# Kernel tuning notes

Hardware: AMD Instinct MI355X
Metric: run time of the kernel (lower is better)

The kernel has to match this reference:

```python
import jax, jax.numpy as jnp
import numpy as np

B, SQ, SK = 32, 512, 512
Q_DIM = 512
K_DIM = 512
H = 8
HD = 64
INNER = H * HD
MAX_POS = 512
SCALE = 1.0 / np.sqrt(HD)


def setup_inputs() -> dict:
    key = jax.random.key(0)
    ks = jax.random.split(key, 10)
    query = jax.random.normal(ks[0], (B, SQ, Q_DIM), dtype=jnp.float32)
    key_t = jax.random.normal(ks[1], (B, SK, K_DIM), dtype=jnp.float32)
    value = jax.random.normal(ks[2], (B, SK, K_DIM), dtype=jnp.float32)
    mask = jax.random.randint(ks[3], (B, SQ, SK), 0, 2, dtype=jnp.int32)
    # learned parameters (Linear weights stored as [in, out]; to_q/k/v have no bias)
    Wq = jax.random.normal(ks[4], (Q_DIM, INNER), dtype=jnp.float32) * 0.02
    Wk = jax.random.normal(ks[5], (K_DIM, INNER), dtype=jnp.float32) * 0.02
    Wv = jax.random.normal(ks[6], (K_DIM, INNER), dtype=jnp.float32) * 0.02
    Wo = jax.random.normal(ks[7], (INNER, Q_DIM), dtype=jnp.float32) * 0.02
    bo = jnp.zeros((Q_DIM,), dtype=jnp.float32)
    rel_pos_emb = jax.random.normal(ks[8], (MAX_POS, MAX_POS), dtype=jnp.float32) * 0.02
    return {"query": query, "key": key_t, "value": value, "mask": mask,
            "Wq": Wq, "Wk": Wk, "Wv": Wv, "Wo": Wo, "bo": bo,
            "rel_pos_emb": rel_pos_emb}


def reference(query, key, value, mask, Wq, Wk, Wv, Wo, bo, rel_pos_emb):
    # Projections (no bias for q/k/v)
    q = query @ Wq   # [B, SQ, INNER]
    k = key @ Wk     # [B, SK, INNER]
    v = value @ Wv   # [B, SK, INNER]
    # split heads -> [B, H, S, HD]
    q = q.reshape(B, SQ, H, HD).transpose(0, 2, 1, 3)
    k = k.reshape(B, SK, H, HD).transpose(0, 2, 1, 3)
    v = v.reshape(B, SK, H, HD).transpose(0, 2, 1, 3)
    # scaled scores + learned relative-position bias (shared across batch/heads)
    scores = jnp.einsum('bhqd,bhkd->bhqk', q, k) * SCALE
    bias = rel_pos_emb[:SQ, :SK]          # [SQ, SK]
    scores = scores + bias[None, None, :, :]
    # additive masking: positions where mask == 0 get -inf
    scores = jnp.where(mask[:, None, :, :] == 0, -jnp.inf, scores)
    attn = jax.nn.softmax(scores, axis=-1)
    # dropout is identity in eval mode (p treated as inference)
    out = jnp.einsum('bhqk,bhkd->bhqd', attn, v)
    out = out.transpose(0, 2, 1, 3).reshape(B, SQ, INNER)
    return out @ Wo + bo
```

## Files before the change

### kernel.cpp

```cpp
#include <hip/hip_runtime.h>
#include <stdint.h>


typedef unsigned short u16;
typedef __attribute__((ext_vector_type(4))) float f32x4;
typedef __attribute__((ext_vector_type(8))) __bf16 bf16x8;
typedef __attribute__((ext_vector_type(4))) unsigned short u16x4;
typedef __attribute__((ext_vector_type(8))) unsigned short u16x8;
typedef __attribute__((ext_vector_type(4))) int i32x4;
typedef __attribute__((ext_vector_type(4))) _Float16 f16x4;
typedef __attribute__((ext_vector_type(8))) _Float16 f16x8;

#define MFMA16(a, b, c) __builtin_amdgcn_mfma_f32_16x16x32_bf16((a), (b), (c), 0, 0, 0)

#define LGKM0_BARRIER()                                        \
  do {                                                         \
    asm volatile("s_waitcnt lgkmcnt(0)" ::: "memory");         \
    __builtin_amdgcn_s_barrier();                              \
    __builtin_amdgcn_sched_barrier(0);                         \
  } while (0)

__device__ __forceinline__ u16 f2bf(float f) {
  unsigned u = __float_as_uint(f);
  u += 0x7fffu + ((u >> 16) & 1u);
  return (u16)(u >> 16);
}
__device__ __forceinline__ float bf2f(u16 h) {
  return __uint_as_float(((unsigned)h) << 16);
}

__device__ __forceinline__ void gl_lds16(const void* g, void* l) {
  __builtin_amdgcn_global_load_lds(
      (const __attribute__((address_space(1))) unsigned int*)g,
      (__attribute__((address_space(3))) unsigned int*)l, 16, 0, 0);
}

__global__ __launch_bounds__(256) void k_prep(
    const float* __restrict__ Wq, const float* __restrict__ Wk,
    const float* __restrict__ Wv, const float* __restrict__ Wo,
    u16* __restrict__ Wt, u16* __restrict__ WoHi, u16* __restrict__ WoLo) {
  int t = blockIdx.x * 256 + threadIdx.x;
  int mat = t >> 15;
  int r = t & 32767;
  int nc = r >> 10, kb = (r >> 6) & 15, lane = r & 63;
  int fr = lane & 15, g = lane >> 4;
  int n = nc * 16 + fr;
  int kbase = kb * 32 + g * 8;
  if (mat < 3) {
    const float* __restrict__ W = (mat == 0) ? Wq : (mat == 1) ? Wk : Wv;
    u16x8 o;
#pragma unroll
    for (int j = 0; j < 8; ++j)
      o[j] = f2bf(W[(size_t)(kbase + j) * 512 + n]);
    *(u16x8*)&Wt[(size_t)mat * 262144 + (size_t)r * 8] = o;
  } else {
    u16x8 oh, ol;
#pragma unroll
    for (int j = 0; j < 8; ++j) {
      float wo = Wo[(size_t)(kbase + j) * 512 + n];
      u16 hi = f2bf(wo);
      oh[j] = hi;
      ol[j] = f2bf(wo - bf2f(hi));
    }
    *(u16x8*)&WoHi[(size_t)r * 8] = oh;
    *(u16x8*)&WoLo[(size_t)r * 8] = ol;
  }
}

__global__ __launch_bounds__(256) void k_cvt(
    const float* __restrict__ Xq, const float* __restrict__ Xk,
    const float* __restrict__ Xv, u16* __restrict__ Xb) {
  const float* __restrict__ src =
      (blockIdx.y == 0) ? Xq : (blockIdx.y == 1) ? Xk : Xv;
  size_t i8 = ((size_t)blockIdx.x * 256 + threadIdx.x) * 8;
  f32x4 v0 = *(const f32x4*)&src[i8];
  f32x4 v1 = *(const f32x4*)&src[i8 + 4];
  u16x8 o;
#pragma unroll
  for (int e = 0; e < 4; ++e) {
    o[e]     = f2bf(v0[e]);
    o[e + 4] = f2bf(v1[e]);
  }
  *(u16x8*)&Xb[(size_t)blockIdx.y * 8388608 + i8] = o;
}

__global__ __launch_bounds__(256) void k_mb(
    const int* __restrict__ mask, const float* __restrict__ bias,
    _Float16* __restrict__ MB) {
  size_t i8 = ((size_t)blockIdx.x * 256 + threadIdx.x) * 8;
  i32x4 m0 = *(const i32x4*)&mask[i8];
  i32x4 m1 = *(const i32x4*)&mask[i8 + 4];
  size_t bi = i8 & 262143;
  f32x4 b0 = *(const f32x4*)&bias[bi];
  f32x4 b1 = *(const f32x4*)&bias[bi + 4];
  const _Float16 MASKED = (_Float16)(-60000.0f);
  f16x8 o;
#pragma unroll
  for (int e = 0; e < 4; ++e) {
    o[e]     = (m0[e] != 0) ? (_Float16)b0[e] : MASKED;
    o[e + 4] = (m1[e] != 0) ? (_Float16)b1[e] : MASKED;
  }
  *(f16x8*)&MB[i8] = o;
}

__global__ __launch_bounds__(256, 4) void k_proj(
    const u16* __restrict__ Xb, const u16* __restrict__ Wt,
    u16* __restrict__ Qb, u16* __restrict__ Kb, u16* __restrict__ Vtb) {
  __shared__ __align__(16) u16 lAb[2][128][64];
  const int mat = blockIdx.z;
  const u16* __restrict__ Ab = Xb + (size_t)mat * 8388608;
  const u16* __restrict__ Bf = Wt + (size_t)mat * 262144;
  const int tid = threadIdx.x, lane = tid & 63, wid = tid >> 6;
  const int wm = wid >> 1, wn = wid & 1;
  const int m0 = blockIdx.y * 128, n0 = blockIdx.x * 128;
  const int fr = lane & 15, g = lane >> 4;

  const int sub = lane >> 3;
  const int xo = ((lane & 7) ^ sub) * 8;
  const int swr = (fr & 7) << 4;

  const int nc0 = (n0 >> 4) + wn * 4;
  const u16* __restrict__ Bq[4];
#pragma unroll
  for (int fn = 0; fn < 4; ++fn)
    Bq[fn] = Bf + (size_t)((nc0 + fn) * 16) * 512 + lane * 8;

  f32x4 acc[4][4] = {};

#pragma unroll
  for (int p = 0; p < 4; ++p) {
    const int rb = p * 32 + wid * 8;
    gl_lds16(Ab + (size_t)(m0 + rb + sub) * 512 + xo, &lAb[0][rb][0]);
  }
  __syncthreads();

  for (int kt = 0; kt < 8; ++kt) {
    const int cur = kt & 1, nxt = cur ^ 1;
    const int k0 = kt * 64;
    bf16x8 bB[2][4];
#pragma unroll
    for (int fn = 0; fn < 4; ++fn) {
      bB[0][fn] = *(const bf16x8*)(Bq[fn] + (size_t)(kt * 2) * 512);
      bB[1][fn] = *(const bf16x8*)(Bq[fn] + (size_t)(kt * 2 + 1) * 512);
    }
    if (kt < 7) {
#pragma unroll
      for (int p = 0; p < 4; ++p) {
        const int rb = p * 32 + wid * 8;
        gl_lds16(Ab + (size_t)(m0 + rb + sub) * 512 + k0 + 64 + xo,
                 &lAb[nxt][rb][0]);
      }
    }
#pragma unroll
    for (int kc = 0; kc < 2; ++kc) {
#pragma unroll
      for (int fm = 0; fm < 4; ++fm) {
        const char* rowb = (const char*)&lAb[cur][wm * 64 + fm * 16 + fr][0];
        bf16x8 af = *(const bf16x8*)(rowb + ((kc * 64 + g * 16) ^ swr));
#pragma unroll
        for (int fn = 0; fn < 4; ++fn)
          acc[fm][fn] = MFMA16(af, bB[kc][fn], acc[fm][fn]);
      }
    }
    __syncthreads();
  }

  if (mat < 2) {
    u16* __restrict__ Out = (mat == 0) ? Qb : Kb;
#pragma unroll
    for (int fm = 0; fm < 4; ++fm) {
#pragma unroll
      for (int fn = 0; fn < 4; ++fn) {
        int gn = n0 + wn * 64 + fn * 16 + fr;
        int hh = gn >> 6, hd = gn & 63;
#pragma unroll
        for (int r = 0; r < 4; ++r) {
          int gm = m0 + wm * 64 + fm * 16 + g * 4 + r;
          int b = gm >> 9, sq = gm & 511;
          Out[(size_t)((b * 8 + hh) * 512 + sq) * 64 + hd] = f2bf(acc[fm][fn][r]);
        }
      }
    }
  } else {
#pragma unroll
    for (int fm = 0; fm < 4; ++fm) {
      int gm0 = m0 + wm * 64 + fm * 16 + g * 4;
      int b = gm0 >> 9, sq0 = gm0 & 511;
#pragma unroll
      for (int fn = 0; fn < 4; ++fn) {
        int gn = n0 + wn * 64 + fn * 16 + fr;
        int hh = gn >> 6, hd = gn & 63;
        u16x4 pv;
        pv[0] = f2bf(acc[fm][fn][0]); pv[1] = f2bf(acc[fm][fn][1]);
        pv[2] = f2bf(acc[fm][fn][2]); pv[3] = f2bf(acc[fm][fn][3]);
        *(u16x4*)&Vtb[(size_t)((b * 8 + hh) * 64 + hd) * 512 + sq0] = pv;
      }
    }
  }
}

__global__ __launch_bounds__(256, 4) void k_attn(
    const u16* __restrict__ Qb, const u16* __restrict__ Kb, const u16* __restrict__ Vtb,
    const _Float16* __restrict__ MB, float* __restrict__ Obuf) {
  __shared__ __align__(16) u16 kbuf[2][64][64];
  __shared__ __align__(16) u16 vbuf[2][64][64];
  __shared__ __align__(16) u16 lP[4][16][64];
  const int tid = threadIdx.x, lane = tid & 63, w = tid >> 6;
  const int orig = blockIdx.x;
  const int xcd = orig & 7, idx = orig >> 3;
  const int qq = idx & 3, h = (idx >> 2) & 7;
  const int b = xcd + 8 * (idx >> 5);
  const int bh = b * 8 + h;
  const int fr = lane & 15, g = lane >> 4;
  const int sq0 = qq * 128 + w * 32;
  const int sw = (fr & 7) << 4;
  const u16* __restrict__ Qh = Qb + (size_t)bh * 32768;
  const u16* __restrict__ Kh = Kb + (size_t)bh * 32768;
  const u16* __restrict__ Vh = Vtb + (size_t)bh * 32768;
  const _Float16* __restrict__ MBr = MB + (size_t)b * 262144 + (size_t)(sq0 + fr) * 512;
  char* lProw = (char*)&lP[w][fr][0];
  const char* kcb;
  const char* vcb;

  const int sub = lane >> 3;
  const int xo = ((lane & 7) ^ sub) * 8;

  bf16x8 qf[2][2];
#pragma unroll
  for (int qfi = 0; qfi < 2; ++qfi)
#pragma unroll
    for (int kc = 0; kc < 2; ++kc)
      qf[qfi][kc] = *(const bf16x8*)&Qh[(size_t)(sq0 + qfi * 16 + fr) * 64 + kc * 32 + g * 8];

  f32x4 oacc[2][4] = {};
  float mrow[2] = {-1e30f, -1e30f}, lrow[2] = {0.f, 0.f};

  {
    if (w < 2) {
      const int rb = w * 32;
      const u16* gs = Kh + (size_t)(rb + sub) * 64 + xo;
#pragma unroll
      for (int i = 0; i < 4; ++i)
        gl_lds16(gs + (size_t)i * 8 * 64, &kbuf[0][rb + i * 8][0]);
    } else {
      const int rb = (w - 2) * 32;
      const u16* gs = Vh + (size_t)(rb + sub) * 512 + xo;
#pragma unroll
      for (int i = 0; i < 4; ++i)
        gl_lds16(gs + (size_t)i * 8 * 512, &vbuf[0][rb + i * 8][0]);
    }
  }
  __syncthreads();

  int cur = 0;
  for (int kt = 0; kt < 8; ++kt) {
    const int sk0 = kt * 64;
    f16x4 mbv[2][4];
#pragma unroll
    for (int qfi = 0; qfi < 2; ++qfi)
#pragma unroll
      for (int fn = 0; fn < 4; ++fn)
        mbv[qfi][fn] = *(const f16x4*)&MBr[(size_t)qfi * 16 * 512 + sk0 + fn * 16 + g * 4];
    if (kt < 7) {
      const int nb = cur ^ 1, sk0n = sk0 + 64;
      if (w < 2) {
        const int rb = w * 32;
        const u16* gs = Kh + (size_t)(sk0n + rb + sub) * 64 + xo;
#pragma unroll
        for (int i = 0; i < 4; ++i)
          gl_lds16(gs + (size_t)i * 8 * 64, &kbuf[nb][rb + i * 8][0]);
      } else {
        const int rb = (w - 2) * 32;
        const u16* gs = Vh + (size_t)(rb + sub) * 512 + sk0n + xo;
#pragma unroll
        for (int i = 0; i < 4; ++i)
          gl_lds16(gs + (size_t)i * 8 * 512, &vbuf[nb][rb + i * 8][0]);
      }
    }
    kcb = (const char*)kbuf[cur];
    vcb = (const char*)vbuf[cur];
    f32x4 sacc[2][4] = {};
#pragma unroll
    for (int fn = 0; fn < 4; ++fn) {
      const int r = fn * 16 + fr;
      bf16x8 kf0 = *(const bf16x8*)(kcb + (size_t)r * 128 + ((0 * 64 + g * 16) ^ sw));
      bf16x8 kf1 = *(const bf16x8*)(kcb + (size_t)r * 128 + ((1 * 64 + g * 16) ^ sw));
      sacc[0][fn] = MFMA16(kf0, qf[0][0], sacc[0][fn]);
      sacc[0][fn] = MFMA16(kf1, qf[0][1], sacc[0][fn]);
      sacc[1][fn] = MFMA16(kf0, qf[1][0], sacc[1][fn]);
      sacc[1][fn] = MFMA16(kf1, qf[1][1], sacc[1][fn]);
    }
#pragma unroll
    for (int qfi = 0; qfi < 2; ++qfi)
#pragma unroll
      for (int fn = 0; fn < 4; ++fn)
#pragma unroll
        for (int r = 0; r < 4; ++r)
          sacc[qfi][fn][r] = sacc[qfi][fn][r] * 0.125f + (float)mbv[qfi][fn][r];

#pragma unroll
    for (int qfi = 0; qfi < 2; ++qfi) {
      float t0 = fmaxf(fmaxf(sacc[qfi][0][0], sacc[qfi][0][1]),
                       fmaxf(sacc[qfi][0][2], sacc[qfi][0][3]));
      float t1 = fmaxf(fmaxf(sacc[qfi][1][0], sacc[qfi][1][1]),
                       fmaxf(sacc[qfi][1][2], sacc[qfi][1][3]));
      float t2 = fmaxf(fmaxf(sacc[qfi][2][0], sacc[qfi][2][1]),
                       fmaxf(sacc[qfi][2][2], sacc[qfi][2][3]));
      float t3 = fmaxf(fmaxf(sacc[qfi][3][0], sacc[qfi][3][1]),
                       fmaxf(sacc[qfi][3][2], sacc[qfi][3][3]));
      float pm = fmaxf(fmaxf(t0, t1), fmaxf(t2, t3));
      pm = fmaxf(pm, __shfl_xor(pm, 16));
      pm = fmaxf(pm, __shfl_xor(pm, 32));
      if (!__all(pm - mrow[qfi] <= 8.0f)) {
        float mn = fmaxf(mrow[qfi], pm);
        float sfac = __expf(mrow[qfi] - mn);
        mrow[qfi] = mn;
        lrow[qfi] *= sfac;
#pragma unroll
        for (int r = 0; r < 4; ++r) {
          float sr = __shfl(sfac, g * 4 + r);
#pragma unroll
          for (int fnh = 0; fnh < 4; ++fnh)
            oacc[qfi][fnh][r] *= sr;
        }
      }
      float ps = 0.f;
#pragma unroll
      for (int fn = 0; fn < 4; ++fn) {
        float p0 = __expf(sacc[qfi][fn][0] - mrow[qfi]);
        float p1 = __expf(sacc[qfi][fn][1] - mrow[qfi]);
        float p2 = __expf(sacc[qfi][fn][2] - mrow[qfi]);
        float p3 = __expf(sacc[qfi][fn][3] - mrow[qfi]);
        ps += (p0 + p1) + (p2 + p3);
        u16x4 pw;
        pw[0] = f2bf(p0); pw[1] = f2bf(p1); pw[2] = f2bf(p2); pw[3] = f2bf(p3);
        *(u16x4*)(lProw + ((fn * 32 + g * 8) ^ sw)) = pw;
      }
      ps += __shfl_xor(ps, 16);
      ps += __shfl_xor(ps, 32);
      lrow[qfi] += ps;
      __builtin_amdgcn_wave_barrier();
#pragma unroll
      for (int kc = 0; kc < 2; ++kc) {
        bf16x8 pf = *(const bf16x8*)(lProw + ((kc * 64 + g * 16) ^ sw));
#pragma unroll
        for (int fnh = 0; fnh < 4; ++fnh) {
          const int vr = fnh * 16 + fr;
          bf16x8 vf = *(const bf16x8*)(vcb + (size_t)vr * 128 + ((kc * 64 + g * 16) ^ sw));
          oacc[qfi][fnh] = MFMA16(pf, vf, oacc[qfi][fnh]);
        }
      }
      __builtin_amdgcn_wave_barrier();
    }
    __syncthreads();
    cur ^= 1;
  }
#pragma unroll
  for (int qfi = 0; qfi < 2; ++qfi) {
#pragma unroll
    for (int r = 0; r < 4; ++r) {
      float lr = __shfl(lrow[qfi], g * 4 + r);
      float inv = 1.0f / lr;
      const int sq = sq0 + qfi * 16 + g * 4 + r;
      float* orow = &Obuf[((size_t)b * 512 + sq) * 512 + h * 64];
#pragma unroll
      for (int fnh = 0; fnh < 4; ++fnh)
        orow[fnh * 16 + fr] = oacc[qfi][fnh][r] * inv;
    }
  }
}

__global__ __launch_bounds__(256, 4) void k_out(
    const float* __restrict__ Oin, const u16* __restrict__ WoHi, const u16* __restrict__ WoLo,
    const float* __restrict__ bo, float* __restrict__ out) {
  __shared__ __align__(16) u16 lAh[2][64][40], lAl[2][64][40];
  const int tid = threadIdx.x, lane = tid & 63, wn = tid >> 6;
  const int m0 = blockIdx.y * 64, n0 = blockIdx.x * 128;
  const int fr = lane & 15, g = lane >> 4;
  const int arow = tid >> 2, acg = tid & 3;
  const float* __restrict__ Ar = &Oin[(size_t)(m0 + arow) * 512 + acg * 8];
  const int nc0 = (n0 >> 4) + wn * 2;
  const u16* __restrict__ Bhp[2];
  const u16* __restrict__ Blp[2];
#pragma unroll
  for (int fn = 0; fn < 2; ++fn) {
    size_t off = (size_t)((nc0 + fn) * 16) * 512 + lane * 8;
    Bhp[fn] = WoHi + off;
    Blp[fn] = WoLo + off;
  }

  f32x4 acc[4][2] = {};
  f32x4 va[2][2];

  {
    f32x4 v0 = *(const f32x4*)&Ar[0];
    f32x4 v1 = *(const f32x4*)&Ar[4];
    va[0][0] = *(const f32x4*)&Ar[32];
    va[0][1] = *(const f32x4*)&Ar[36];
    u16x8 hv, lv;
#pragma unroll
    for (int e = 0; e < 4; ++e) {
      u16 hb0 = f2bf(v0[e]);
      u16 hb1 = f2bf(v1[e]);
      hv[e] = hb0; hv[e + 4] = hb1;
      lv[e] = f2bf(v0[e] - bf2f(hb0));
      lv[e + 4] = f2bf(v1[e] - bf2f(hb1));
    }
    *(u16x8*)&lAh[0][arow][acg * 8] = hv;
    *(u16x8*)&lAl[0][arow][acg * 8] = lv;
  }
  LGKM0_BARRIER();

#pragma unroll
  for (int kt = 0; kt < 16; ++kt) {
    const int cur = kt & 1, nxt = cur ^ 1;
    bf16x8 bh[2], bl[2];
#pragma unroll
    for (int fn = 0; fn < 2; ++fn) {
      bh[fn] = *(const bf16x8*)(Bhp[fn] + (size_t)kt * 512);
      bl[fn] = *(const bf16x8*)(Blp[fn] + (size_t)kt * 512);
    }
    if (kt < 14) {
      va[nxt][0] = *(const f32x4*)&Ar[(kt + 2) * 32];
      va[nxt][1] = *(const f32x4*)&Ar[(kt + 2) * 32 + 4];
    }
#pragma unroll
    for (int fm = 0; fm < 4; ++fm) {
      bf16x8 ah = *(const bf16x8*)&lAh[cur][fm * 16 + fr][g * 8];
      bf16x8 al = *(const bf16x8*)&lAl[cur][fm * 16 + fr][g * 8];
#pragma unroll
      for (int fn = 0; fn < 2; ++fn) {
        acc[fm][fn] = MFMA16(ah, bh[fn], acc[fm][fn]);
        acc[fm][fn] = MFMA16(ah, bl[fn], acc[fm][fn]);
        acc[fm][fn] = MFMA16(al, bh[fn], acc[fm][fn]);
      }
    }
    if (kt < 15) {
      u16x8 hv, lv;
#pragma unroll
      for (int e = 0; e < 4; ++e) {
        u16 hb0 = f2bf(va[cur][0][e]);
        u16 hb1 = f2bf(va[cur][1][e]);
        hv[e] = hb0; hv[e + 4] = hb1;
        lv[e] = f2bf(va[cur][0][e] - bf2f(hb0));
        lv[e + 4] = f2bf(va[cur][1][e] - bf2f(hb1));
      }
      *(u16x8*)&lAh[nxt][arow][acg * 8] = hv;
      *(u16x8*)&lAl[nxt][arow][acg * 8] = lv;
    }
    LGKM0_BARRIER();
  }

#pragma unroll
  for (int fm = 0; fm < 4; ++fm) {
#pragma unroll
    for (int fn = 0; fn < 2; ++fn) {
      int gn = n0 + wn * 32 + fn * 16 + fr;
      float bv = bo[gn];
#pragma unroll
      for (int r = 0; r < 4; ++r) {
        int gm = m0 + fm * 16 + g * 4 + r;
        out[(size_t)gm * 512 + gn] = acc[fm][fn][r] + bv;
      }
    }
  }
}

extern "C" void kernel_launch(void* const* d_in, const int* in_sizes, int n_in,
                              void* d_out, int out_size, void* d_ws, size_t ws_size,
                              hipStream_t stream) {
  (void)in_sizes; (void)n_in; (void)out_size; (void)ws_size;
  const float* query = (const float*)d_in[0];
  const float* key_t = (const float*)d_in[1];
  const float* value = (const float*)d_in[2];
  const int*   mask  = (const int*)d_in[3];
  const float* Wq    = (const float*)d_in[4];
  const float* Wk    = (const float*)d_in[5];
  const float* Wv    = (const float*)d_in[6];
  const float* Wo    = (const float*)d_in[7];
  const float* bo    = (const float*)d_in[8];
  const float* bias  = (const float*)d_in[9];
  float* out = (float*)d_out;

  char* p = (char*)d_ws;
  u16* Wt   = (u16*)p; p += (size_t)3 * 512 * 512 * 2;
  u16* WoHi = (u16*)p; p += (size_t)512 * 512 * 2;
  u16* WoLo = (u16*)p; p += (size_t)512 * 512 * 2;
  u16* Qb   = (u16*)p; p += (size_t)32 * 8 * 512 * 64 * 2;
  u16* Kb   = (u16*)p; p += (size_t)32 * 8 * 512 * 64 * 2;
  u16* Vtb  = (u16*)p; p += (size_t)32 * 8 * 512 * 64 * 2;
  u16* Xb = (u16*)p;
  float* Obuf = (float*)p;
  _Float16* MBp = (_Float16*)(p + (size_t)32 * 512 * 512 * 4);

  k_prep<<<512, 256, 0, stream>>>(Wq, Wk, Wv, Wo, Wt, WoHi, WoLo);
  k_cvt<<<dim3(4096, 3), 256, 0, stream>>>(query, key_t, value, Xb);
  k_proj<<<dim3(4, 128, 3), 256, 0, stream>>>(Xb, Wt, Qb, Kb, Vtb);
  k_mb<<<4096, 256, 0, stream>>>(mask, bias, MBp);
  k_attn<<<1024, 256, 0, stream>>>(Qb, Kb, Vtb, MBp, Obuf);
  k_out<<<dim3(4, 256), 256, 0, stream>>>(Obuf, WoHi, WoLo, bo, out);
}
```

Measured before the change: 182.4 us.

## Split attention block into eight waves each handling sixteen query rows

Each attention block now runs 512 threads (8 waves), and each wave owns 16 query rows instead of 32. The K/V tile loads are spread over eight waves, and the P scratch buffer grows to one slice per wave. The aim is more waves in flight to hide latency and lower register pressure per wave. In exchange, each K/V tile read from LDS is reused across half as many rows, so LDS read traffic per MFMA goes up, and block-wide barriers now synchronise more waves.

```diff
diff --git a/kernel.cpp b/kernel.cpp
--- a/kernel.cpp
+++ b/kernel.cpp
@@ -199,12 +199,12 @@
   }
 }
 
-__global__ __launch_bounds__(256, 4) void k_attn(
+__global__ __launch_bounds__(512, 6) void k_attn(
     const u16* __restrict__ Qb, const u16* __restrict__ Kb, const u16* __restrict__ Vtb,
     const _Float16* __restrict__ MB, float* __restrict__ Obuf) {
   __shared__ __align__(16) u16 kbuf[2][64][64];
   __shared__ __align__(16) u16 vbuf[2][64][64];
-  __shared__ __align__(16) u16 lP[4][16][64];
+  __shared__ __align__(16) u16 lP[8][16][64];
   const int tid = threadIdx.x, lane = tid & 63, w = tid >> 6;
   const int orig = blockIdx.x;
   const int xcd = orig & 7, idx = orig >> 3;
@@ -212,161 +212,134 @@
   const int b = xcd + 8 * (idx >> 5);
   const int bh = b * 8 + h;
   const int fr = lane & 15, g = lane >> 4;
-  const int sq0 = qq * 128 + w * 32;
+  const int sq0 = qq * 128 + w * 16;
   const int sw = (fr & 7) << 4;
   const u16* __restrict__ Qh = Qb + (size_t)bh * 32768;
   const u16* __restrict__ Kh = Kb + (size_t)bh * 32768;
   const u16* __restrict__ Vh = Vtb + (size_t)bh * 32768;
   const _Float16* __restrict__ MBr = MB + (size_t)b * 262144 + (size_t)(sq0 + fr) * 512;
   char* lProw = (char*)&lP[w][fr][0];
-  const char* kcb;
-  const char* vcb;
 
   const int sub = lane >> 3;
   const int xo = ((lane & 7) ^ sub) * 8;
 
-  bf16x8 qf[2][2];
-#pragma unroll
-  for (int qfi = 0; qfi < 2; ++qfi)
-#pragma unroll
-    for (int kc = 0; kc < 2; ++kc)
-      qf[qfi][kc] = *(const bf16x8*)&Qh[(size_t)(sq0 + qfi * 16 + fr) * 64 + kc * 32 + g * 8];
-
-  f32x4 oacc[2][4] = {};
-  float mrow[2] = {-1e30f, -1e30f}, lrow[2] = {0.f, 0.f};
-
-  {
-    if (w < 2) {
-      const int rb = w * 32;
-      const u16* gs = Kh + (size_t)(rb + sub) * 64 + xo;
-#pragma unroll
-      for (int i = 0; i < 4; ++i)
-        gl_lds16(gs + (size_t)i * 8 * 64, &kbuf[0][rb + i * 8][0]);
-    } else {
-      const int rb = (w - 2) * 32;
-      const u16* gs = Vh + (size_t)(rb + sub) * 512 + xo;
-#pragma unroll
-      for (int i = 0; i < 4; ++i)
-        gl_lds16(gs + (size_t)i * 8 * 512, &vbuf[0][rb + i * 8][0]);
-    }
+  bf16x8 qf[2];
+  qf[0] = *(const bf16x8*)&Qh[(size_t)(sq0 + fr) * 64 + g * 8];
+  qf[1] = *(const bf16x8*)&Qh[(size_t)(sq0 + fr) * 64 + 32 + g * 8];
+
+  f32x4 oacc[4] = {};
+  float mrow = -1e30f, lrow = 0.f;
+
+  if (w < 4) {
+    const int rb = w * 16;
+    const u16* gs = Kh + (size_t)(rb + sub) * 64 + xo;
+    gl_lds16(gs, &kbuf[0][rb][0]);
+    gl_lds16(gs + 8 * 64, &kbuf[0][rb + 8][0]);
+  } else {
+    const int rb = (w - 4) * 16;
+    const u16* gs = Vh + (size_t)(rb + sub) * 512 + xo;
+    gl_lds16(gs, &vbuf[0][rb][0]);
+    gl_lds16(gs + 8 * 512, &vbuf[0][rb + 8][0]);
   }
   __syncthreads();
 
   int cur = 0;
   for (int kt = 0; kt < 8; ++kt) {
     const int sk0 = kt * 64;
-    f16x4 mbv[2][4];
-#pragma unroll
-    for (int qfi = 0; qfi < 2; ++qfi)
-#pragma unroll
-      for (int fn = 0; fn < 4; ++fn)
-        mbv[qfi][fn] = *(const f16x4*)&MBr[(size_t)qfi * 16 * 512 + sk0 + fn * 16 + g * 4];
+    f16x4 mbv[4];
+#pragma unroll
+    for (int fn = 0; fn < 4; ++fn)
+      mbv[fn] = *(const f16x4*)&MBr[sk0 + fn * 16 + g * 4];
     if (kt < 7) {
       const int nb = cur ^ 1, sk0n = sk0 + 64;
-      if (w < 2) {
-        const int rb = w * 32;
+      if (w < 4) {
+        const int rb = w * 16;
         const u16* gs = Kh + (size_t)(sk0n + rb + sub) * 64 + xo;
-#pragma unroll
-        for (int i = 0; i < 4; ++i)
-          gl_lds16(gs + (size_t)i * 8 * 64, &kbuf[nb][rb + i * 8][0]);
+        gl_lds16(gs, &kbuf[nb][rb][0]);
+        gl_lds16(gs + 8 * 64, &kbuf[nb][rb + 8][0]);
       } else {
-        const int rb = (w - 2) * 32;
+        const int rb = (w - 4) * 16;
         const u16* gs = Vh + (size_t)(rb + sub) * 512 + sk0n + xo;
-#pragma unroll
-        for (int i = 0; i < 4; ++i)
-          gl_lds16(gs + (size_t)i * 8 * 512, &vbuf[nb][rb + i * 8][0]);
-      }
-    }
-    kcb = (const char*)kbuf[cur];
-    vcb = (const char*)vbuf[cur];
-    f32x4 sacc[2][4] = {};
+        gl_lds16(gs, &vbuf[nb][rb][0]);
+        gl_lds16(gs + 8 * 512, &vbuf[nb][rb + 8][0]);
+      }
+    }
+    const char* kcb = (const char*)kbuf[cur];
+    const char* vcb = (const char*)vbuf[cur];
+    f32x4 sacc[4] = {};
 #pragma unroll
     for (int fn = 0; fn < 4; ++fn) {
       const int r = fn * 16 + fr;
       bf16x8 kf0 = *(const bf16x8*)(kcb + (size_t)r * 128 + ((0 * 64 + g * 16) ^ sw));
       bf16x8 kf1 = *(const bf16x8*)(kcb + (size_t)r * 128 + ((1 * 64 + g * 16) ^ sw));
-      sacc[0][fn] = MFMA16(kf0, qf[0][0], sacc[0][fn]);
-      sacc[0][fn] = MFMA16(kf1, qf[0][1], sacc[0][fn]);
-      sacc[1][fn] = MFMA16(kf0, qf[1][0], sacc[1][fn]);
-      sacc[1][fn] = MFMA16(kf1, qf[1][1], sacc[1][fn]);
-    }
-#pragma unroll
-    for (int qfi = 0; qfi < 2; ++qfi)
-#pragma unroll
-      for (int fn = 0; fn < 4; ++fn)
-#pragma unroll
-        for (int r = 0; r < 4; ++r)
-          sacc[qfi][fn][r] = sacc[qfi][fn][r] * 0.125f + (float)mbv[qfi][fn][r];
-
-#pragma unroll
-    for (int qfi = 0; qfi < 2; ++qfi) {
-      float t0 = fmaxf(fmaxf(sacc[qfi][0][0], sacc[qfi][0][1]),
-                       fmaxf(sacc[qfi][0][2], sacc[qfi][0][3]));
-      float t1 = fmaxf(fmaxf(sacc[qfi][1][0], sacc[qfi][1][1]),
-                       fmaxf(sacc[qfi][1][2], sacc[qfi][1][3]));
-      float t2 = fmaxf(fmaxf(sacc[qfi][2][0], sacc[qfi][2][1]),
-                       fmaxf(sacc[qfi][2][2], sacc[qfi][2][3]));
-      float t3 = fmaxf(fmaxf(sacc[qfi][3][0], sacc[qfi][3][1]),
-                       fmaxf(sacc[qfi][3][2], sacc[qfi][3][3]));
-      float pm = fmaxf(fmaxf(t0, t1), fmaxf(t2, t3));
-      pm = fmaxf(pm, __shfl_xor(pm, 16));
-      pm = fmaxf(pm, __shfl_xor(pm, 32));
-      if (!__all(pm - mrow[qfi] <= 8.0f)) {
-        float mn = fmaxf(mrow[qfi], pm);
-        float sfac = __expf(mrow[qfi] - mn);
-        mrow[qfi] = mn;
-        lrow[qfi] *= sfac;
-#pragma unroll
-        for (int r = 0; r < 4; ++r) {
-          float sr = __shfl(sfac, g * 4 + r);
-#pragma unroll
-          for (int fnh = 0; fnh < 4; ++fnh)
-            oacc[qfi][fnh][r] *= sr;
-        }
-      }
-      float ps = 0.f;
-#pragma unroll
-      for (int fn = 0; fn < 4; ++fn) {
-        float p0 = __expf(sacc[qfi][fn][0] - mrow[qfi]);
-        float p1 = __expf(sacc[qfi][fn][1] - mrow[qfi]);
-        float p2 = __expf(sacc[qfi][fn][2] - mrow[qfi]);
-        float p3 = __expf(sacc[qfi][fn][3] - mrow[qfi]);
-        ps += (p0 + p1) + (p2 + p3);
-        u16x4 pw;
-        pw[0] = f2bf(p0); pw[1] = f2bf(p1); pw[2] = f2bf(p2); pw[3] = f2bf(p3);
-        *(u16x4*)(lProw + ((fn * 32 + g * 8) ^ sw)) = pw;
-      }
-      ps += __shfl_xor(ps, 16);
-      ps += __shfl_xor(ps, 32);
-      lrow[qfi] += ps;
-      __builtin_amdgcn_wave_barrier();
-#pragma unroll
-      for (int kc = 0; kc < 2; ++kc) {
-        bf16x8 pf = *(const bf16x8*)(lProw + ((kc * 64 + g * 16) ^ sw));
-#pragma unroll
-        for (int fnh = 0; fnh < 4; ++fnh) {
-          const int vr = fnh * 16 + fr;
-          bf16x8 vf = *(const bf16x8*)(vcb + (size_t)vr * 128 + ((kc * 64 + g * 16) ^ sw));
-          oacc[qfi][fnh] = MFMA16(pf, vf, oacc[qfi][fnh]);
-        }
-      }
-      __builtin_amdgcn_wave_barrier();
-    }
+      sacc[fn] = MFMA16(kf0, qf[0], sacc[fn]);
+      sacc[fn] = MFMA16(kf1, qf[1], sacc[fn]);
+    }
+#pragma unroll
+    for (int fn = 0; fn < 4; ++fn)
+#pragma unroll
+      for (int r = 0; r < 4; ++r)
+        sacc[fn][r] = sacc[fn][r] * 0.125f + (float)mbv[fn][r];
+
+    float t0 = fmaxf(fmaxf(sacc[0][0], sacc[0][1]), fmaxf(sacc[0][2], sacc[0][3]));
+    float t1 = fmaxf(fmaxf(sacc[1][0], sacc[1][1]), fmaxf(sacc[1][2], sacc[1][3]));
+    float t2 = fmaxf(fmaxf(sacc[2][0], sacc[2][1]), fmaxf(sacc[2][2], sacc[2][3]));
+    float t3 = fmaxf(fmaxf(sacc[3][0], sacc[3][1]), fmaxf(sacc[3][2], sacc[3][3]));
+    float pm = fmaxf(fmaxf(t0, t1), fmaxf(t2, t3));
+    pm = fmaxf(pm, __shfl_xor(pm, 16));
+    pm = fmaxf(pm, __shfl_xor(pm, 32));
+    if (!__all(pm - mrow <= 8.0f)) {
+      float mn = fmaxf(mrow, pm);
+      float sfac = __expf(mrow - mn);
+      mrow = mn;
+      lrow *= sfac;
+#pragma unroll
+      for (int r = 0; r < 4; ++r) {
+        float sr = __shfl(sfac, g * 4 + r);
+#pragma unroll
+        for (int fnh = 0; fnh < 4; ++fnh)
+          oacc[fnh][r] *= sr;
+      }
+    }
+    float ps = 0.f;
+#pragma unroll
+    for (int fn = 0; fn < 4; ++fn) {
+      float p0 = __expf(sacc[fn][0] - mrow);
+      float p1 = __expf(sacc[fn][1] - mrow);
+      float p2 = __expf(sacc[fn][2] - mrow);
+      float p3 = __expf(sacc[fn][3] - mrow);
+      ps += (p0 + p1) + (p2 + p3);
+      u16x4 pw;
+      pw[0] = f2bf(p0); pw[1] = f2bf(p1); pw[2] = f2bf(p2); pw[3] = f2bf(p3);
+      *(u16x4*)(lProw + ((fn * 32 + g * 8) ^ sw)) = pw;
+    }
+    ps += __shfl_xor(ps, 16);
+    ps += __shfl_xor(ps, 32);
+    lrow += ps;
+    __builtin_amdgcn_wave_barrier();
+#pragma unroll
+    for (int kc = 0; kc < 2; ++kc) {
+      bf16x8 pf = *(const bf16x8*)(lProw + ((kc * 64 + g * 16) ^ sw));
+#pragma unroll
+      for (int fnh = 0; fnh < 4; ++fnh) {
+        const int vr = fnh * 16 + fr;
+        bf16x8 vf = *(const bf16x8*)(vcb + (size_t)vr * 128 + ((kc * 64 + g * 16) ^ sw));
+        oacc[fnh] = MFMA16(pf, vf, oacc[fnh]);
+      }
+    }
+    __builtin_amdgcn_wave_barrier();
     __syncthreads();
     cur ^= 1;
   }
 #pragma unroll
-  for (int qfi = 0; qfi < 2; ++qfi) {
-#pragma unroll
-    for (int r = 0; r < 4; ++r) {
-      float lr = __shfl(lrow[qfi], g * 4 + r);
-      float inv = 1.0f / lr;
-      const int sq = sq0 + qfi * 16 + g * 4 + r;
-      float* orow = &Obuf[((size_t)b * 512 + sq) * 512 + h * 64];
-#pragma unroll
-      for (int fnh = 0; fnh < 4; ++fnh)
-        orow[fnh * 16 + fr] = oacc[qfi][fnh][r] * inv;
-    }
+  for (int r = 0; r < 4; ++r) {
+    float lr = __shfl(lrow, g * 4 + r);
+    float inv = 1.0f / lr;
+    const int sq = sq0 + g * 4 + r;
+    float* orow = &Obuf[((size_t)b * 512 + sq) * 512 + h * 64];
+#pragma unroll
+    for (int fnh = 0; fnh < 4; ++fnh)
+      orow[fnh * 16 + fr] = oacc[fnh][r] * inv;
   }
 }
 
@@ -497,6 +470,6 @@
   k_cvt<<<dim3(4096, 3), 256, 0, stream>>>(query, key_t, value, Xb);
   k_proj<<<dim3(4, 128, 3), 256, 0, stream>>>(Xb, Wt, Qb, Kb, Vtb);
   k_mb<<<4096, 256, 0, stream>>>(mask, bias, MBp);
-  k_attn<<<1024, 256, 0, stream>>>(Qb, Kb, Vtb, MBp, Obuf);
+  k_attn<<<1024, 512, 0, stream>>>(Qb, Kb, Vtb, MBp, Obuf);
   k_out<<<dim3(4, 256), 256, 0, stream>>>(Obuf, WoHi, WoLo, bo, out);
 }
```

Result: slower. 188.3 us (+3.2%).

## Emit bf16 hi/lo attention output and stream it into k_out via LDS DMA

Applied to the files above, without the earlier changes.

The attention kernel now writes its output as two bf16 planes (high part and residual) instead of fp32, so the split-precision conversion happens once in k_attn rather than inside the output projection. k_out then loads these planes directly into swizzled LDS with global_load_lds, processes 64-wide K tiles (8 iterations instead of 16), and uses plain __syncthreads instead of the lgkm-wait barrier. This removes the per-iteration register conversion and VGPR staging in k_out and keeps intermediate traffic the same size. It depends on the hi+lo bf16 split keeping enough accuracy, and the k_attn epilogue now does more stores per element.

```diff
diff --git a/kernel.cpp b/kernel.cpp
--- a/kernel.cpp
+++ b/kernel.cpp
@@ -12,13 +12,6 @@
 typedef __attribute__((ext_vector_type(8))) _Float16 f16x8;
 
 #define MFMA16(a, b, c) __builtin_amdgcn_mfma_f32_16x16x32_bf16((a), (b), (c), 0, 0, 0)
-
-#define LGKM0_BARRIER()                                        \
-  do {                                                         \
-    asm volatile("s_waitcnt lgkmcnt(0)" ::: "memory");         \
-    __builtin_amdgcn_s_barrier();                              \
-    __builtin_amdgcn_sched_barrier(0);                         \
-  } while (0)
 
 __device__ __forceinline__ u16 f2bf(float f) {
   unsigned u = __float_as_uint(f);
@@ -201,7 +194,8 @@
 
 __global__ __launch_bounds__(256, 4) void k_attn(
     const u16* __restrict__ Qb, const u16* __restrict__ Kb, const u16* __restrict__ Vtb,
-    const _Float16* __restrict__ MB, float* __restrict__ Obuf) {
+    const _Float16* __restrict__ MB,
+    u16* __restrict__ Ohi, u16* __restrict__ Olo) {
   __shared__ __align__(16) u16 kbuf[2][64][64];
   __shared__ __align__(16) u16 vbuf[2][64][64];
   __shared__ __align__(16) u16 lP[4][16][64];
@@ -219,8 +213,6 @@
   const u16* __restrict__ Vh = Vtb + (size_t)bh * 32768;
   const _Float16* __restrict__ MBr = MB + (size_t)b * 262144 + (size_t)(sq0 + fr) * 512;
   char* lProw = (char*)&lP[w][fr][0];
-  const char* kcb;
-  const char* vcb;
 
   const int sub = lane >> 3;
   const int xo = ((lane & 7) ^ sub) * 8;
@@ -277,8 +269,8 @@
           gl_lds16(gs + (size_t)i * 8 * 512, &vbuf[nb][rb + i * 8][0]);
       }
     }
-    kcb = (const char*)kbuf[cur];
-    vcb = (const char*)vbuf[cur];
+    const char* kcb = (const char*)kbuf[cur];
+    const char* vcb = (const char*)vbuf[cur];
     f32x4 sacc[2][4] = {};
 #pragma unroll
     for (int fn = 0; fn < 4; ++fn) {
@@ -362,23 +354,33 @@
       float lr = __shfl(lrow[qfi], g * 4 + r);
       float inv = 1.0f / lr;
       const int sq = sq0 + qfi * 16 + g * 4 + r;
-      float* orow = &Obuf[((size_t)b * 512 + sq) * 512 + h * 64];
-#pragma unroll
-      for (int fnh = 0; fnh < 4; ++fnh)
-        orow[fnh * 16 + fr] = oacc[qfi][fnh][r] * inv;
+      const size_t base = ((size_t)b * 512 + sq) * 512 + h * 64;
+#pragma unroll
+      for (int fnh = 0; fnh < 4; ++fnh) {
+        float o = oacc[qfi][fnh][r] * inv;
+        u16 oh = f2bf(o);
+        Ohi[base + fnh * 16 + fr] = oh;
+        Olo[base + fnh * 16 + fr] = f2bf(o - bf2f(oh));
+      }
     }
   }
 }
 
 __global__ __launch_bounds__(256, 4) void k_out(
-    const float* __restrict__ Oin, const u16* __restrict__ WoHi, const u16* __restrict__ WoLo,
+    const u16* __restrict__ Ohi, const u16* __restrict__ Olo,
+    const u16* __restrict__ WoHi, const u16* __restrict__ WoLo,
     const float* __restrict__ bo, float* __restrict__ out) {
-  __shared__ __align__(16) u16 lAh[2][64][40], lAl[2][64][40];
-  const int tid = threadIdx.x, lane = tid & 63, wn = tid >> 6;
+  __shared__ __align__(16) u16 lAh[2][64][64];
+  __shared__ __align__(16) u16 lAl[2][64][64];
+  const int tid = threadIdx.x, lane = tid & 63, w = tid >> 6;
+  const int wn = w;
   const int m0 = blockIdx.y * 64, n0 = blockIdx.x * 128;
   const int fr = lane & 15, g = lane >> 4;
-  const int arow = tid >> 2, acg = tid & 3;
-  const float* __restrict__ Ar = &Oin[(size_t)(m0 + arow) * 512 + acg * 8];
+
+  const int sub = lane >> 3;
+  const int xo = ((lane & 7) ^ sub) * 8;
+  const int swr = (fr & 7) << 4;
+
   const int nc0 = (n0 >> 4) + wn * 2;
   const u16* __restrict__ Bhp[2];
   const u16* __restrict__ Blp[2];
@@ -390,65 +392,52 @@
   }
 
   f32x4 acc[4][2] = {};
-  f32x4 va[2][2];
 
   {
-    f32x4 v0 = *(const f32x4*)&Ar[0];
-    f32x4 v1 = *(const f32x4*)&Ar[4];
-    va[0][0] = *(const f32x4*)&Ar[32];
-    va[0][1] = *(const f32x4*)&Ar[36];
-    u16x8 hv, lv;
-#pragma unroll
-    for (int e = 0; e < 4; ++e) {
-      u16 hb0 = f2bf(v0[e]);
-      u16 hb1 = f2bf(v1[e]);
-      hv[e] = hb0; hv[e + 4] = hb1;
-      lv[e] = f2bf(v0[e] - bf2f(hb0));
-      lv[e + 4] = f2bf(v1[e] - bf2f(hb1));
-    }
-    *(u16x8*)&lAh[0][arow][acg * 8] = hv;
-    *(u16x8*)&lAl[0][arow][acg * 8] = lv;
-  }
-  LGKM0_BARRIER();
-
-#pragma unroll
-  for (int kt = 0; kt < 16; ++kt) {
+    const int rb = w * 16;
+    gl_lds16(Ohi + (size_t)(m0 + rb + sub) * 512 + xo,     &lAh[0][rb][0]);
+    gl_lds16(Ohi + (size_t)(m0 + rb + 8 + sub) * 512 + xo, &lAh[0][rb + 8][0]);
+    gl_lds16(Olo + (size_t)(m0 + rb + sub) * 512 + xo,     &lAl[0][rb][0]);
+    gl_lds16(Olo + (size_t)(m0 + rb + 8 + sub) * 512 + xo, &lAl[0][rb + 8][0]);
+  }
+  __syncthreads();
+
+  for (int kt = 0; kt < 8; ++kt) {
     const int cur = kt & 1, nxt = cur ^ 1;
-    bf16x8 bh[2], bl[2];
-#pragma unroll
-    for (int fn = 0; fn < 2; ++fn) {
-      bh[fn] = *(const bf16x8*)(Bhp[fn] + (size_t)kt * 512);
-      bl[fn] = *(const bf16x8*)(Blp[fn] + (size_t)kt * 512);
-    }
-    if (kt < 14) {
-      va[nxt][0] = *(const f32x4*)&Ar[(kt + 2) * 32];
-      va[nxt][1] = *(const f32x4*)&Ar[(kt + 2) * 32 + 4];
-    }
-#pragma unroll
-    for (int fm = 0; fm < 4; ++fm) {
-      bf16x8 ah = *(const bf16x8*)&lAh[cur][fm * 16 + fr][g * 8];
-      bf16x8 al = *(const bf16x8*)&lAl[cur][fm * 16 + fr][g * 8];
+    const int k0 = kt * 64;
+    bf16x8 bh[2][2], bl[2][2];
+#pragma unroll
+    for (int kc = 0; kc < 2; ++kc)
 #pragma unroll
       for (int fn = 0; fn < 2; ++fn) {
-        acc[fm][fn] = MFMA16(ah, bh[fn], acc[fm][fn]);
-        acc[fm][fn] = MFMA16(ah, bl[fn], acc[fm][fn]);
-        acc[fm][fn] = MFMA16(al, bh[fn], acc[fm][fn]);
-      }
-    }
-    if (kt < 15) {
-      u16x8 hv, lv;
-#pragma unroll
-      for (int e = 0; e < 4; ++e) {
-        u16 hb0 = f2bf(va[cur][0][e]);
-        u16 hb1 = f2bf(va[cur][1][e]);
-        hv[e] = hb0; hv[e + 4] = hb1;
-        lv[e] = f2bf(va[cur][0][e] - bf2f(hb0));
-        lv[e + 4] = f2bf(va[cur][1][e] - bf2f(hb1));
-      }
-      *(u16x8*)&lAh[nxt][arow][acg * 8] = hv;
-      *(u16x8*)&lAl[nxt][arow][acg * 8] = lv;
-    }
-    LGKM0_BARRIER();
+        bh[kc][fn] = *(const bf16x8*)(Bhp[fn] + (size_t)(kt * 2 + kc) * 512);
+        bl[kc][fn] = *(const bf16x8*)(Blp[fn] + (size_t)(kt * 2 + kc) * 512);
+      }
+    if (kt < 7) {
+      const int rb = w * 16;
+      gl_lds16(Ohi + (size_t)(m0 + rb + sub) * 512 + k0 + 64 + xo,     &lAh[nxt][rb][0]);
+      gl_lds16(Ohi + (size_t)(m0 + rb + 8 + sub) * 512 + k0 + 64 + xo, &lAh[nxt][rb + 8][0]);
+      gl_lds16(Olo + (size_t)(m0 + rb + sub) * 512 + k0 + 64 + xo,     &lAl[nxt][rb][0]);
+      gl_lds16(Olo + (size_t)(m0 + rb + 8 + sub) * 512 + k0 + 64 + xo, &lAl[nxt][rb + 8][0]);
+    }
+#pragma unroll
+    for (int kc = 0; kc < 2; ++kc) {
+#pragma unroll
+      for (int fm = 0; fm < 4; ++fm) {
+        const char* rowh = (const char*)&lAh[cur][fm * 16 + fr][0];
+        const char* rowl = (const char*)&lAl[cur][fm * 16 + fr][0];
+        const int bc = (kc * 64 + g * 16) ^ swr;
+        bf16x8 ah = *(const bf16x8*)(rowh + bc);
+        bf16x8 al = *(const bf16x8*)(rowl + bc);
+#pragma unroll
+        for (int fn = 0; fn < 2; ++fn) {
+          acc[fm][fn] = MFMA16(ah, bh[kc][fn], acc[fm][fn]);
+          acc[fm][fn] = MFMA16(ah, bl[kc][fn], acc[fm][fn]);
+          acc[fm][fn] = MFMA16(al, bh[kc][fn], acc[fm][fn]);
+        }
+      }
+    }
+    __syncthreads();
   }
 
 #pragma unroll
@@ -490,13 +479,14 @@
   u16* Kb   = (u16*)p; p += (size_t)32 * 8 * 512 * 64 * 2;
   u16* Vtb  = (u16*)p; p += (size_t)32 * 8 * 512 * 64 * 2;
   u16* Xb = (u16*)p;
-  float* Obuf = (float*)p;
-  _Float16* MBp = (_Float16*)(p + (size_t)32 * 512 * 512 * 4);
+  u16* Ohi = (u16*)p;
+  u16* Olo = (u16*)(p + (size_t)16384 * 512 * 2);
+  _Float16* MBp = (_Float16*)(p + (size_t)2 * 16384 * 512 * 2);
 
   k_prep<<<512, 256, 0, stream>>>(Wq, Wk, Wv, Wo, Wt, WoHi, WoLo);
   k_cvt<<<dim3(4096, 3), 256, 0, stream>>>(query, key_t, value, Xb);
   k_proj<<<dim3(4, 128, 3), 256, 0, stream>>>(Xb, Wt, Qb, Kb, Vtb);
   k_mb<<<4096, 256, 0, stream>>>(mask, bias, MBp);
-  k_attn<<<1024, 256, 0, stream>>>(Qb, Kb, Vtb, MBp, Obuf);
-  k_out<<<dim3(4, 256), 256, 0, stream>>>(Obuf, WoHi, WoLo, bo, out);
-}
+  k_attn<<<1024, 256, 0, stream>>>(Qb, Kb, Vtb, MBp, Ohi, Olo);
+  k_out<<<dim3(4, 256), 256, 0, stream>>>(Ohi, Olo, WoHi, WoLo, bo, out);
+}
```

Result: faster. 175.0 us (-4.0%).
